# Kernel optimization log

Measured on AMD Instinct MI355X. Metric: run time of the kernel, lower is better.

## Reference

```python
import jax, jax.numpy as jnp
import numpy as np

N_NODES = 50000
N_EDGES = 1600000
IN_DIM = 128
OUT_DIM = 128
PRELU_INIT = 0.25
EPS = 1e-8


def setup_inputs() -> dict:
    key = jax.random.key(0)
    k_seq, k_w, k_r, k_c = jax.random.split(key, 4)
    seq = jax.random.normal(k_seq, (N_NODES, IN_DIM), dtype=jnp.float32)
    # xavier_normal_ with gain=1.414 on a [out_dim, in_dim] Linear weight
    std = 1.414 * np.sqrt(2.0 / (IN_DIM + OUT_DIM))
    W = jax.random.normal(k_w, (OUT_DIM, IN_DIM), dtype=jnp.float32) * std
    alpha = jnp.full((1,), PRELU_INIT, dtype=jnp.float32)
    rows = jax.random.randint(k_r, (N_EDGES,), 0, N_NODES)  # destination node per edge
    cols = jax.random.randint(k_c, (N_EDGES,), 0, N_NODES)  # source node per edge
    return {"seq": seq, "W": W, "alpha": alpha, "rows": rows, "cols": cols}


def reference(seq, W, alpha, rows, cols):
    # fc: seq @ W.T  -> [N, out_dim]
    seq_fts = seq @ W.T
    # spmm(adj, seq_fts): sum features of source nodes into destination rows
    agg = jax.ops.segment_sum(seq_fts[cols], rows, num_segments=N_NODES)
    # spmm(adj, ones): per-row degree
    deg = jax.ops.segment_sum(jnp.ones((rows.shape[0],), dtype=seq.dtype), rows,
                              num_segments=N_NODES)
    out = agg / (deg[:, None] + EPS)
    # PReLU with single shared parameter alpha
    return jnp.where(out >= 0, out, alpha[0] * out)
```

## Files before the change

### kernel.cpp

```cpp
#include <hip/hip_runtime.h>

#define N_NODES 50000
#define N_EDGES 1600000
#define DIM 128
#define NPB 64
#define NB 782
#define SEG_CAP 2560
#define EPB 2048
#define NBLK 782
#define EPT (EPB / 256)
#define HPS 784


typedef __attribute__((ext_vector_type(8))) short bf16x8;
typedef __attribute__((ext_vector_type(4))) float f32x4;

__device__ __forceinline__ unsigned short f2bf_rne(float f) {
    unsigned b = __float_as_uint(f);
    return (unsigned short)((b + 0x7FFFu + ((b >> 16) & 1u)) >> 16);
}

__global__ __launch_bounds__(256) void p1_k(const int* __restrict__ rows,
                                            const int* __restrict__ cols,
                                            unsigned* __restrict__ packed,
                                            unsigned short* __restrict__ hp,
                                            const float* __restrict__ seq,
                                            unsigned short* __restrict__ seq16,
                                            const float* __restrict__ W,
                                            unsigned short* __restrict__ W16) {
    __shared__ int lh[NB];
    __shared__ int lcur[NB];
    __shared__ unsigned stg[EPB];
    __shared__ int wtot[4];
    int t = threadIdx.x, blk = blockIdx.x;
    for (int i = t; i < NB; i += 256) lh[i] = 0;
    __syncthreads();
    int base = blk * EPB;
    int er[EPT], ec[EPT];
#pragma unroll
    for (int it = 0; it < EPT; ++it) {
        int e = base + it * 256 + t;
        if (e < N_EDGES) {
            er[it] = rows[e];
            ec[it] = cols[e];
            atomicAdd(&lh[er[it] >> 6], 1);
        } else {
            er[it] = -1;
            ec[it] = 0;
        }
    }
    const float4* s4 = (const float4*)seq;
    ushort4* d4 = (ushort4*)seq16;
    for (int i = blk * 256 + t; i < N_NODES * DIM / 4; i += NBLK * 256) {
        float4 v = s4[i];
        ushort4 o;
        o.x = f2bf_rne(v.x);
        o.y = f2bf_rne(v.y);
        o.z = f2bf_rne(v.z);
        o.w = f2bf_rne(v.w);
        d4[i] = o;
    }
    if (blk == 0) {
        const float4* w4 = (const float4*)W;
        ushort4* o4 = (ushort4*)W16;
        for (int i = t; i < DIM * DIM / 4; i += 256) {
            float4 v = w4[i];
            ushort4 o;
            o.x = f2bf_rne(v.x);
            o.y = f2bf_rne(v.y);
            o.z = f2bf_rne(v.z);
            o.w = f2bf_rne(v.w);
            o4[i] = o;
        }
    }
    __syncthreads();
    int myb = t * 4;
    int c0 = 0, c1 = 0, c2 = 0, c3 = 0, s = 0;
    if (myb < NB) {
        c0 = lh[myb];
        c1 = (myb + 1 < NB) ? lh[myb + 1] : 0;
        c2 = (myb + 2 < NB) ? lh[myb + 2] : 0;
        c3 = (myb + 3 < NB) ? lh[myb + 3] : 0;
        s = c0 + c1 + c2 + c3;
    }
    int x = s;
#pragma unroll
    for (int o = 1; o < 64; o <<= 1) {
        int u = __shfl_up(x, o);
        if ((t & 63) >= o) x += u;
    }
    if ((t & 63) == 63) wtot[t >> 6] = x;
    __syncthreads();
    int off = 0;
    for (int ww = 0; ww < (t >> 6); ++ww) off += wtot[ww];
    if (myb < NB) {
        int r = off + x - s;
        unsigned short* hrow = hp + blk * HPS;
        lcur[myb] = r; r += c0; hrow[myb] = (unsigned short)r;
        if (myb + 1 < NB) { lcur[myb + 1] = r; r += c1; hrow[myb + 1] = (unsigned short)r; }
        if (myb + 2 < NB) { lcur[myb + 2] = r; r += c2; hrow[myb + 2] = (unsigned short)r; }
        if (myb + 3 < NB) { lcur[myb + 3] = r; r += c3; hrow[myb + 3] = (unsigned short)r; }
    }
    __syncthreads();
#pragma unroll
    for (int it = 0; it < EPT; ++it) {
        int r = er[it];
        if (r >= 0) {
            int pos = atomicAdd(&lcur[r >> 6], 1);
            stg[pos] = ((unsigned)(r & 63) << 16) | (unsigned)ec[it];
        }
    }
    __syncthreads();
    const uint4* sv = (const uint4*)stg;
    uint4* dv = (uint4*)(packed + blk * EPB);
    for (int i = t; i < EPB / 4; i += 256) dv[i] = sv[i];
}

#define ACC(u)                                      \
    {                                               \
        f0 += __uint_as_float((u).x << 16);         \
        f1 += __uint_as_float((u).x & 0xFFFF0000u); \
        f2 += __uint_as_float((u).y << 16);         \
        f3 += __uint_as_float((u).y & 0xFFFF0000u); \
    }

__global__ __launch_bounds__(512, 8) void aggemm_k(const uint2* __restrict__ seqD,
                                                   const unsigned* __restrict__ packed,
                                                   const unsigned short* __restrict__ hp,
                                                   const unsigned short* __restrict__ W16,
                                                   const float* __restrict__ alpha_p,
                                                   float* __restrict__ out) {
    __shared__ unsigned rawl[SEG_CAP];
    __shared__ unsigned colsl[SEG_CAP];
    __shared__ unsigned meanL[NPB * 68];
    __shared__ int hist[NPB];
    __shared__ int lbase[NPB];
    __shared__ int lcur[NPB];
    __shared__ int rawn;
    int b = blockIdx.x, t = threadIdx.x;
    if (t == 0) rawn = 0;
    if (t < NPB) hist[t] = 0;
    __syncthreads();
    for (int blk = t; blk < NBLK; blk += 512) {
        int hbase = blk * HPS;
        int end = hp[hbase + b];
        int start = b ? hp[hbase + b - 1] : 0;
        int cnt = end - start;
        if (cnt > 0) {
            int pos = atomicAdd(&rawn, cnt);
            if (pos + cnt <= SEG_CAP) {
                const unsigned* src = packed + blk * EPB + start;
                for (int i = 0; i < cnt; ++i) {
                    unsigned p = src[i];
                    rawl[pos + i] = p;
                    atomicAdd(&hist[p >> 16], 1);
                }
            }
        }
    }
    __syncthreads();
    int n = min(rawn, SEG_CAP);
    if (t < NPB) {
        int v = hist[t], x = v;
#pragma unroll
        for (int o = 1; o < 64; o <<= 1) {
            int u = __shfl_up(x, o);
            if (t >= o) x += u;
        }
        lbase[t] = x - v;
        lcur[t] = x - v;
    }
    __syncthreads();
    for (int i = t; i < n; i += 512) {
        unsigned p = rawl[i];
        int pos = atomicAdd(&lcur[p >> 16], 1);
        colsl[pos] = p & 0xFFFFu;
    }
    __syncthreads();

    int w = t >> 6, lane = t & 63;
    int h = lane >> 5, l = lane & 31;
#pragma unroll 1
    for (int ii = 0; ii < 8; ++ii) {
        int ln = w * 8 + ii;
        int node = b * NPB + ln;
        int base = lbase[ln], d = hist[ln];
        float f0 = 0.f, f1 = 0.f, f2 = 0.f, f3 = 0.f;
        if (node < N_NODES) {
            int j = 0;
            for (; j + 16 <= d; j += 16) {
                unsigned c0 = colsl[base + j + h];
                unsigned c1 = colsl[base + j + 2 + h];
                unsigned c2 = colsl[base + j + 4 + h];
                unsigned c3 = colsl[base + j + 6 + h];
                unsigned c4 = colsl[base + j + 8 + h];
                unsigned c5 = colsl[base + j + 10 + h];
                unsigned c6 = colsl[base + j + 12 + h];
                unsigned c7 = colsl[base + j + 14 + h];
                uint2 u0 = seqD[c0 * 32 + l];
                uint2 u1 = seqD[c1 * 32 + l];
                uint2 u2 = seqD[c2 * 32 + l];
                uint2 u3 = seqD[c3 * 32 + l];
                uint2 u4 = seqD[c4 * 32 + l];
                uint2 u5 = seqD[c5 * 32 + l];
                uint2 u6 = seqD[c6 * 32 + l];
                uint2 u7 = seqD[c7 * 32 + l];
                ACC(u0) ACC(u1) ACC(u2) ACC(u3)
                ACC(u4) ACC(u5) ACC(u6) ACC(u7)
            }
            if (j + 8 <= d) {
                unsigned c0 = colsl[base + j + h];
                unsigned c1 = colsl[base + j + 2 + h];
                unsigned c2 = colsl[base + j + 4 + h];
                unsigned c3 = colsl[base + j + 6 + h];
                uint2 u0 = seqD[c0 * 32 + l];
                uint2 u1 = seqD[c1 * 32 + l];
                uint2 u2 = seqD[c2 * 32 + l];
                uint2 u3 = seqD[c3 * 32 + l];
                ACC(u0) ACC(u1) ACC(u2) ACC(u3)
                j += 8;
            }
            for (; j < d; j += 2) {
                int e = j + h;
                if (e < d) {
                    uint2 u = seqD[colsl[base + e] * 32 + l];
                    ACC(u)
                }
            }
        }
        f0 += __shfl_xor(f0, 32);
        f1 += __shfl_xor(f1, 32);
        f2 += __shfl_xor(f2, 32);
        f3 += __shfl_xor(f3, 32);
        float inv = 1.0f / ((float)d + 1e-8f);
        float va = (h ? f2 : f0) * inv;
        float vb = (h ? f3 : f1) * inv;
        unsigned rx = (unsigned)f2bf_rne(va);
        unsigned ry = (unsigned)f2bf_rne(vb);
        meanL[ln * 68 + 2 * l + h] = (node < N_NODES) ? (rx | (ry << 16)) : 0u;
    }
    __syncthreads();

    int lane15 = lane & 15, quad = lane >> 4;
    int col = w * 16 + lane15;
    bf16x8 bfr[4];
#pragma unroll
    for (int kc = 0; kc < 4; ++kc)
        bfr[kc] = *(const bf16x8*)(W16 + col * 128 + kc * 32 + quad * 8);
    float al = alpha_p[0];
    const unsigned short* mbase = (const unsigned short*)meanL;

#pragma unroll
    for (int m = 0; m < 4; ++m) {
        f32x4 acc = {0.f, 0.f, 0.f, 0.f};
#pragma unroll
        for (int kc = 0; kc < 4; ++kc) {
            bf16x8 a = *(const bf16x8*)(mbase + (m * 16 + lane15) * 136 + kc * 32 + quad * 8);
            acc = __builtin_amdgcn_mfma_f32_16x16x32_bf16(a, bfr[kc], acc, 0, 0, 0);
        }
        int row0 = b * NPB + m * 16 + quad * 4;
#pragma unroll
        for (int r = 0; r < 4; ++r) {
            int row = row0 + r;
            if (row < N_NODES) {
                float v = acc[r];
                v = v >= 0.f ? v : al * v;
                out[row * DIM + w * 16 + lane15] = v;
            }
        }
    }
}

extern "C" void kernel_launch(void* const* d_in, const int* in_sizes, int n_in,
                              void* d_out, int out_size, void* d_ws, size_t ws_size,
                              hipStream_t stream) {
    const float* seq = (const float*)d_in[0];
    const float* W = (const float*)d_in[1];
    const float* alpha = (const float*)d_in[2];
    const int* rows = (const int*)d_in[3];
    const int* cols = (const int*)d_in[4];
    float* out = (float*)d_out;

    char* ws = (char*)d_ws;
    unsigned short* seq16 = (unsigned short*)(ws);
    unsigned short* W16 = (unsigned short*)(ws + 12800000);
    unsigned* packed = (unsigned*)(ws + 12832768);
    unsigned short* hp = (unsigned short*)(ws + 19238912);

    p1_k<<<NBLK, 256, 0, stream>>>(rows, cols, packed, hp, seq, seq16, W, W16);
    aggemm_k<<<NB, 512, 0, stream>>>((const uint2*)seq16, packed, hp, W16, alpha, out);
}
```

Before: 164.2 us.

## Halve edge partition count and parallelize segment gather via prefix-sum index list

The partition kernel now uses 391 blocks of 512 threads with 4096 edges each, halving the number of per-block segments the aggregation kernel must gather. In the aggregation kernel, the serial per-thread copy loop with an atomic cursor is replaced by a block-wide prefix sum over segment counts, an index list built in shared memory, and a fully parallel coalesced gather of packed edges. Shared memory for the raw edge list, the index list and the mean matrix is overlaid into one buffer to cut LDS use. This aims to remove the long serial, uncoalesced per-thread loops and atomic contention, at the cost of an extra sync and indirection through the index list.

```diff
diff --git a/kernel.cpp b/kernel.cpp
--- a/kernel.cpp
+++ b/kernel.cpp
@@ -6,9 +6,9 @@
 #define NPB 64
 #define NB 782
 #define SEG_CAP 2560
-#define EPB 2048
-#define NBLK 782
-#define EPT (EPB / 256)
+#define EPB 4096
+#define NBLK 391
+#define EPT (EPB / 512)
 #define HPS 784
 
 
@@ -20,7 +20,7 @@
     return (unsigned short)((b + 0x7FFFu + ((b >> 16) & 1u)) >> 16);
 }
 
-__global__ __launch_bounds__(256) void p1_k(const int* __restrict__ rows,
+__global__ __launch_bounds__(512) void p1_k(const int* __restrict__ rows,
                                             const int* __restrict__ cols,
                                             unsigned* __restrict__ packed,
                                             unsigned short* __restrict__ hp,
@@ -31,15 +31,15 @@
     __shared__ int lh[NB];
     __shared__ int lcur[NB];
     __shared__ unsigned stg[EPB];
-    __shared__ int wtot[4];
+    __shared__ int wtot[8];
     int t = threadIdx.x, blk = blockIdx.x;
-    for (int i = t; i < NB; i += 256) lh[i] = 0;
+    for (int i = t; i < NB; i += 512) lh[i] = 0;
     __syncthreads();
     int base = blk * EPB;
     int er[EPT], ec[EPT];
 #pragma unroll
     for (int it = 0; it < EPT; ++it) {
-        int e = base + it * 256 + t;
+        int e = base + it * 512 + t;
         if (e < N_EDGES) {
             er[it] = rows[e];
             ec[it] = cols[e];
@@ -51,7 +51,7 @@
     }
     const float4* s4 = (const float4*)seq;
     ushort4* d4 = (ushort4*)seq16;
-    for (int i = blk * 256 + t; i < N_NODES * DIM / 4; i += NBLK * 256) {
+    for (int i = blk * 512 + t; i < N_NODES * DIM / 4; i += NBLK * 512) {
         float4 v = s4[i];
         ushort4 o;
         o.x = f2bf_rne(v.x);
@@ -63,7 +63,7 @@
     if (blk == 0) {
         const float4* w4 = (const float4*)W;
         ushort4* o4 = (ushort4*)W16;
-        for (int i = t; i < DIM * DIM / 4; i += 256) {
+        for (int i = t; i < DIM * DIM / 4; i += 512) {
             float4 v = w4[i];
             ushort4 o;
             o.x = f2bf_rne(v.x);
@@ -74,14 +74,12 @@
         }
     }
     __syncthreads();
-    int myb = t * 4;
-    int c0 = 0, c1 = 0, c2 = 0, c3 = 0, s = 0;
+    int myb = 2 * t;
+    int c0 = 0, c1 = 0, s = 0;
     if (myb < NB) {
         c0 = lh[myb];
         c1 = (myb + 1 < NB) ? lh[myb + 1] : 0;
-        c2 = (myb + 2 < NB) ? lh[myb + 2] : 0;
-        c3 = (myb + 3 < NB) ? lh[myb + 3] : 0;
-        s = c0 + c1 + c2 + c3;
+        s = c0 + c1;
     }
     int x = s;
 #pragma unroll
@@ -98,8 +96,6 @@
         unsigned short* hrow = hp + blk * HPS;
         lcur[myb] = r; r += c0; hrow[myb] = (unsigned short)r;
         if (myb + 1 < NB) { lcur[myb + 1] = r; r += c1; hrow[myb + 1] = (unsigned short)r; }
-        if (myb + 2 < NB) { lcur[myb + 2] = r; r += c2; hrow[myb + 2] = (unsigned short)r; }
-        if (myb + 3 < NB) { lcur[myb + 3] = r; r += c3; hrow[myb + 3] = (unsigned short)r; }
     }
     __syncthreads();
 #pragma unroll
@@ -113,7 +109,7 @@
     __syncthreads();
     const uint4* sv = (const uint4*)stg;
     uint4* dv = (uint4*)(packed + blk * EPB);
-    for (int i = t; i < EPB / 4; i += 256) dv[i] = sv[i];
+    for (int i = t; i < EPB / 4; i += 512) dv[i] = sv[i];
 }
 
 #define ACC(u)                                      \
@@ -130,45 +126,59 @@
                                                    const unsigned short* __restrict__ W16,
                                                    const float* __restrict__ alpha_p,
                                                    float* __restrict__ out) {
-    __shared__ unsigned rawl[SEG_CAP];
     __shared__ unsigned colsl[SEG_CAP];
-    __shared__ unsigned meanL[NPB * 68];
+    __shared__ alignas(16) char ovl[20480];
     __shared__ int hist[NPB];
     __shared__ int lbase[NPB];
     __shared__ int lcur[NPB];
+    __shared__ int wsum[8];
     __shared__ int rawn;
+    unsigned* rawl = (unsigned*)ovl;
+    int* srcidx = (int*)(ovl + 10240);
     int b = blockIdx.x, t = threadIdx.x;
-    if (t == 0) rawn = 0;
     if (t < NPB) hist[t] = 0;
-    __syncthreads();
-    for (int blk = t; blk < NBLK; blk += 512) {
-        int hbase = blk * HPS;
-        int end = hp[hbase + b];
-        int start = b ? hp[hbase + b - 1] : 0;
-        int cnt = end - start;
-        if (cnt > 0) {
-            int pos = atomicAdd(&rawn, cnt);
-            if (pos + cnt <= SEG_CAP) {
-                const unsigned* src = packed + blk * EPB + start;
-                for (int i = 0; i < cnt; ++i) {
-                    unsigned p = src[i];
-                    rawl[pos + i] = p;
-                    atomicAdd(&hist[p >> 16], 1);
-                }
-            }
-        }
+
+    int cnt = 0, start = 0;
+    if (t < NBLK) {
+        const unsigned short* hrow = hp + t * HPS;
+        int e16 = hrow[b];
+        start = b ? hrow[b - 1] : 0;
+        cnt = e16 - start;
+    }
+    int x = cnt;
+#pragma unroll
+    for (int o = 1; o < 64; o <<= 1) {
+        int u = __shfl_up(x, o);
+        if ((t & 63) >= o) x += u;
+    }
+    if ((t & 63) == 63) wsum[t >> 6] = x;
+    __syncthreads();
+    int off = 0;
+    for (int ww = 0; ww < (t >> 6); ++ww) off += wsum[ww];
+    int rp = off + x - cnt;
+    if (t == 511) rawn = off + x;
+    if (cnt > 0) {
+        if (rp + cnt > SEG_CAP) cnt = SEG_CAP - rp;
+        int s0 = t * EPB + start;
+        for (int k = 0; k < cnt; ++k) srcidx[rp + k] = s0 + k;
     }
     __syncthreads();
     int n = min(rawn, SEG_CAP);
+    for (int i = t; i < n; i += 512) {
+        unsigned p = packed[srcidx[i]];
+        rawl[i] = p;
+        atomicAdd(&hist[p >> 16], 1);
+    }
+    __syncthreads();
     if (t < NPB) {
-        int v = hist[t], x = v;
+        int v = hist[t], xx = v;
 #pragma unroll
         for (int o = 1; o < 64; o <<= 1) {
-            int u = __shfl_up(x, o);
-            if (t >= o) x += u;
-        }
-        lbase[t] = x - v;
-        lcur[t] = x - v;
+            int u = __shfl_up(xx, o);
+            if (t >= o) xx += u;
+        }
+        lbase[t] = xx - v;
+        lcur[t] = xx - v;
     }
     __syncthreads();
     for (int i = t; i < n; i += 512) {
@@ -178,6 +188,7 @@
     }
     __syncthreads();
 
+    unsigned* meanL = (unsigned*)ovl;
     int w = t >> 6, lane = t & 63;
     int h = lane >> 5, l = lane & 31;
 #pragma unroll 1
@@ -248,7 +259,7 @@
     for (int kc = 0; kc < 4; ++kc)
         bfr[kc] = *(const bf16x8*)(W16 + col * 128 + kc * 32 + quad * 8);
     float al = alpha_p[0];
-    const unsigned short* mbase = (const unsigned short*)meanL;
+    const unsigned short* mbase = (const unsigned short*)ovl;
 
 #pragma unroll
     for (int m = 0; m < 4; ++m) {
@@ -287,6 +298,6 @@
     unsigned* packed = (unsigned*)(ws + 12832768);
     unsigned short* hp = (unsigned short*)(ws + 19238912);
 
-    p1_k<<<NBLK, 256, 0, stream>>>(rows, cols, packed, hp, seq, seq16, W, W16);
+    p1_k<<<NBLK, 512, 0, stream>>>(rows, cols, packed, hp, seq, seq16, W, W16);
     aggemm_k<<<NB, 512, 0, stream>>>((const uint2*)seq16, packed, hp, W16, alpha, out);
 }
```

After: 158.1 us. 1.04x faster.
